# Kernel optimization log

Hardware: AMD Instinct MI355X
Metric: run time of the kernel (lower is better)

The kernel has to match this reference:

```python
import jax, jax.numpy as jnp
import numpy as np

B, L, D, H = 2, 2048, 1024, 16
HD = D // H


def setup_inputs() -> dict:
    key = jax.random.key(0)
    ks = jax.random.split(key, 5)
    # xavier-uniform-ish scale for DxD linears
    scale = float(np.sqrt(6.0 / (D + D)))
    def lin_w(k):
        return jax.random.uniform(k, (D, D), jnp.float32, -scale, scale)
    return {
        "x": jax.random.normal(ks[0], (B, L, D), jnp.float32),
        "wq": lin_w(ks[1]), "bq": jnp.zeros((D,), jnp.float32),
        "wk": lin_w(ks[2]), "bk": jnp.zeros((D,), jnp.float32),
        "wv": lin_w(ks[3]), "bv": jnp.zeros((D,), jnp.float32),
        "wo": lin_w(ks[4]), "bo": jnp.zeros((D,), jnp.float32),
    }


def reference(x, wq, bq, wk, bk, wv, bv, wo, bo):
    b, l, d = x.shape
    # projections: torch Linear is x @ W.T + b
    def split_heads(t):
        return t.reshape(b, l, H, HD).transpose(0, 2, 1, 3)  # (B,H,L,HD)
    Q = split_heads(x @ wq.T + bq)
    K = split_heads(x @ wk.T + bk)
    V = split_heads(x @ wv.T + bv)
    scores = jnp.einsum("bhqd,bhkd->bhqk", Q, K) / jnp.sqrt(jnp.asarray(HD, x.dtype))
    attn = jax.nn.softmax(scores, axis=-1)  # (B,H,L,L)
    out = jnp.einsum("bhqk,bhkd->bhqd", attn, V)
    out = out.transpose(0, 2, 1, 3).reshape(b, l, d)
    return out @ wo.T + bo
```

## Files before the change

### kernel.cpp

```cpp
#include <hip/hip_runtime.h>
#include <hip/hip_bf16.h>
#include <cstdint>

#define LEN   2048
#define DMODEL 1024
#define NH    16
#define HD    64
#define BH    32
#define MROWS 4096

typedef __attribute__((ext_vector_type(8))) short bf16x8;
typedef __attribute__((ext_vector_type(4))) float f32x4;
typedef __attribute__((ext_vector_type(16))) float f32x16;
typedef unsigned int u32;

__device__ __forceinline__ void gload_lds16(const void* g, void* l) {
    __builtin_amdgcn_global_load_lds(
        (const __attribute__((address_space(1))) u32*)g,
        (__attribute__((address_space(3))) u32*)l, 16, 0, 0);
}

__device__ __forceinline__ unsigned short bfb(float f) {
    __hip_bfloat16 h = __float2bfloat16(f);
    return *reinterpret_cast<unsigned short*>(&h);
}

__device__ __forceinline__ u32 pk2(float lo, float hi) {
    return (u32)bfb(lo) | ((u32)bfb(hi) << 16);
}

__global__ void cast_all_k(const float* __restrict__ x,
                           const float* __restrict__ wq, const float* __restrict__ wk,
                           const float* __restrict__ wv, const float* __restrict__ wo,
                           __hip_bfloat16* __restrict__ x_bf,
                           __hip_bfloat16* __restrict__ wqkv,
                           __hip_bfloat16* __restrict__ wo_bf) {
    constexpr int XC = 1048576;
    constexpr int WC = 262144;
    constexpr int TC = XC + 4 * WC;
    int stride = gridDim.x * blockDim.x;
    for (int i = blockIdx.x * blockDim.x + threadIdx.x; i < TC; i += stride) {
        const float* src; __hip_bfloat16* dst; int so, do_;
        if (i < XC) { src = x; dst = x_bf; so = i; do_ = i; }
        else {
            int j = i - XC, w = j >> 18, o = j & (WC - 1);
            src = w == 0 ? wq : (w == 1 ? wk : (w == 2 ? wv : wo));
            so = o;
            if (w < 3) { dst = wqkv; do_ = j; }
            else       { dst = wo_bf; do_ = o; }
        }
        float4 v = reinterpret_cast<const float4*>(src)[so];
        ushort4 p;
        p.x = bfb(v.x); p.y = bfb(v.y); p.z = bfb(v.z); p.w = bfb(v.w);
        reinterpret_cast<ushort4*>(dst)[do_] = p;
    }
}

__global__ __launch_bounds__(256) void gemm_qkv(
    const __hip_bfloat16* __restrict__ A,
    const __hip_bfloat16* __restrict__ Bw,
    const float* __restrict__ bq, const float* __restrict__ bk,
    const float* __restrict__ bv,
    __hip_bfloat16* __restrict__ Qb, __hip_bfloat16* __restrict__ Kb,
    __hip_bfloat16* __restrict__ VTb) {
    constexpr int Kd = DMODEL;
    __shared__ __hip_bfloat16 As[128 * 32];
    __shared__ __hip_bfloat16 Bs[128 * 32];
    const int lin = blockIdx.x;
    const int wg = (lin & 7) * 96 + (lin >> 3);
    const int by = wg / 24, bx = wg % 24;
    const int tid = threadIdx.x;
    const int wave = tid >> 6, lane = tid & 63;
    const int lg = lane >> 4, lr = lane & 15;
    const int wr = wave >> 1, wc = wave & 1;
    const __hip_bfloat16* Ab = A + (size_t)by * 128 * Kd;
    const __hip_bfloat16* Bb = Bw + (size_t)bx * 128 * Kd;
    f32x4 acc[4][4] = {};
    for (int kt = 0; kt < Kd / 32; ++kt) {
#pragma unroll
        for (int i = 0; i < 2; ++i) {
            int c = tid + i * 256;
            int row = c >> 2, c4 = c & 3;
            gload_lds16(Ab + (size_t)row * Kd + kt * 32 + c4 * 8, &As[c * 8]);
        }
#pragma unroll
        for (int i = 0; i < 2; ++i) {
            int c = tid + i * 256;
            int row = c >> 2, c4 = c & 3;
            gload_lds16(Bb + (size_t)row * Kd + kt * 32 + c4 * 8, &Bs[c * 8]);
        }
        __syncthreads();
        bf16x8 af[4], bfr[4];
#pragma unroll
        for (int m = 0; m < 4; ++m)
            af[m] = *(const bf16x8*)&As[(wr * 64 + m * 16 + lr) * 32 + lg * 8];
#pragma unroll
        for (int n = 0; n < 4; ++n)
            bfr[n] = *(const bf16x8*)&Bs[(wc * 64 + n * 16 + lr) * 32 + lg * 8];
        __builtin_amdgcn_s_setprio(1);
#pragma unroll
        for (int m = 0; m < 4; ++m)
#pragma unroll
            for (int n = 0; n < 4; ++n)
                acc[m][n] = __builtin_amdgcn_mfma_f32_16x16x32_bf16(
                    af[m], bfr[n], acc[m][n], 0, 0, 0);
        __builtin_amdgcn_s_setprio(0);
        __syncthreads();
    }
    const int sel = (bx * 128) >> 10;
    const float* bp = sel == 0 ? bq : (sel == 1 ? bk : bv);
    __hip_bfloat16* dst = sel == 0 ? Qb : (sel == 1 ? Kb : VTb);
#pragma unroll
    for (int m = 0; m < 4; ++m)
#pragma unroll
        for (int n = 0; n < 4; ++n)
#pragma unroll
            for (int r = 0; r < 4; ++r) {
                int gm = by * 128 + wr * 64 + m * 16 + lg * 4 + r;
                int gn = bx * 128 + wc * 64 + n * 16 + lr;
                int nn = gn & (DMODEL - 1);
                float v = acc[m][n][r] + bp[nn];
                int bb = gm >> 11, l = gm & (LEN - 1);
                int h = nn >> 6, hd = nn & (HD - 1);
                size_t addr = (sel < 2)
                    ? ((((size_t)bb * NH + h) * LEN + l) * HD + hd)
                    : ((((size_t)bb * NH + h) * HD + hd) * LEN + l);
                dst[addr] = __float2bfloat16(v);
            }
}

#define SC 0.18033688f
__global__ __launch_bounds__(256) void attn_fwd(
    const __hip_bfloat16* __restrict__ Qb,
    const __hip_bfloat16* __restrict__ Kb,
    const __hip_bfloat16* __restrict__ VTb,
    __hip_bfloat16* __restrict__ Ob) {
    const int lin = blockIdx.x;
    const int wg = (lin & 7) * 64 + (lin >> 3);
    const int bh = wg >> 4;
    const int qt = wg & 15;
    const int b = bh >> 4, h = bh & (NH - 1);
    const int tid = threadIdx.x;
    const int wave = tid >> 6, lane = tid & 63;
    const int l31 = lane & 31, hi = lane >> 5;
    const int qw = qt * 128 + wave * 32;
    const __hip_bfloat16* Qp = Qb + ((size_t)bh * LEN + qw) * HD;
    const __hip_bfloat16* Kp = Kb + (size_t)bh * LEN * HD;
    const __hip_bfloat16* Vp = VTb + (size_t)bh * HD * LEN;

    __shared__ __hip_bfloat16 Ks[2][64 * 64];
    __shared__ __hip_bfloat16 Vs[2][64 * 64];
    __shared__ __hip_bfloat16 Pl[4][32][72];
    __hip_bfloat16* prow = &Pl[wave][l31][0];

    const int c0 = tid, c1 = tid + 256;
    const int r0 = c0 >> 3, j0 = (c0 & 7) ^ (r0 & 7);
    const int r1 = c1 >> 3, j1 = (c1 & 7) ^ (r1 & 7);
    const __hip_bfloat16* kg0 = Kp + (size_t)r0 * HD + j0 * 8;
    const __hip_bfloat16* kg1 = Kp + (size_t)r1 * HD + j1 * 8;
    const __hip_bfloat16* vg0 = Vp + (size_t)r0 * LEN + j0 * 8;
    const __hip_bfloat16* vg1 = Vp + (size_t)r1 * LEN + j1 * 8;

    bf16x8 qf[4];
#pragma unroll
    for (int ks = 0; ks < 4; ++ks)
        qf[ks] = *(const bf16x8*)(Qp + l31 * HD + ks * 16 + hi * 8);

    float m_i = -INFINITY;
    float l_i = 0.f;
    f32x16 o[2] = {};

    gload_lds16(kg0, &Ks[0][c0 * 8]);
    gload_lds16(kg1, &Ks[0][c1 * 8]);
    gload_lds16(vg0, &Vs[0][c0 * 8]);
    gload_lds16(vg1, &Vs[0][c1 * 8]);
    __syncthreads();

    const int swz = l31 & 7;
    constexpr int NT = LEN / 64;
    for (int kt = 0; kt < NT; ++kt) {
        const int cb = kt & 1, nb = cb ^ 1;
        if (kt + 1 < NT) {
            size_t ko = (size_t)(kt + 1) * 64 * HD;
            size_t vo = (size_t)(kt + 1) * 64;
            gload_lds16(kg0 + ko, &Ks[nb][c0 * 8]);
            gload_lds16(kg1 + ko, &Ks[nb][c1 * 8]);
            gload_lds16(vg0 + vo, &Vs[nb][c0 * 8]);
            gload_lds16(vg1 + vo, &Vs[nb][c1 * 8]);
        }
        const __hip_bfloat16* ksp = Ks[cb];
        const __hip_bfloat16* vsp = Vs[cb];
        f32x16 s0 = {}, s1 = {};
        __builtin_amdgcn_s_setprio(1);
#pragma unroll
        for (int ks = 0; ks < 4; ++ks) {
            int ch = ((ks << 1) + hi);
            bf16x8 kf0 = *(const bf16x8*)&ksp[l31 * 64 + (ch ^ swz) * 8];
            bf16x8 kf1 = *(const bf16x8*)&ksp[(32 + l31) * 64 + (ch ^ swz) * 8];
            s0 = __builtin_amdgcn_mfma_f32_32x32x16_bf16(kf0, qf[ks], s0, 0, 0, 0);
            s1 = __builtin_amdgcn_mfma_f32_32x32x16_bf16(kf1, qf[ks], s1, 0, 0, 0);
        }
        __builtin_amdgcn_s_setprio(0);
        float mx[16];
#pragma unroll
        for (int r = 0; r < 16; ++r) mx[r] = fmaxf(s0[r], s1[r]);
#pragma unroll
        for (int st = 8; st > 0; st >>= 1)
#pragma unroll
            for (int r = 0; r < 8; ++r)
                if (r < st) mx[r] = fmaxf(mx[r], mx[r + st]);
        float tmax = fmaxf(mx[0], __shfl_xor(mx[0], 32, 64));
        float pmax = tmax * SC;
        if (__any(pmax > m_i + 8.f)) {
            float mnew = fmaxf(m_i, pmax);
            float corr = exp2f(m_i - mnew);
            m_i = mnew;
            l_i *= corr;
#pragma unroll
            for (int r = 0; r < 16; ++r) {
                float cr = __shfl(corr, (r & 3) + 8 * (r >> 2) + 4 * hi, 32);
                o[0][r] *= cr;
                o[1][r] *= cr;
            }
        }
#pragma unroll
        for (int r = 0; r < 16; ++r) {
            s0[r] = exp2f(s0[r] * SC - m_i);
            s1[r] = exp2f(s1[r] * SC - m_i);
        }
        float sm[16];
#pragma unroll
        for (int r = 0; r < 16; ++r) sm[r] = s0[r] + s1[r];
#pragma unroll
        for (int st = 8; st > 0; st >>= 1)
#pragma unroll
            for (int r = 0; r < 8; ++r)
                if (r < st) sm[r] += sm[r + st];
        l_i += sm[0] + __shfl_xor(sm[0], 32, 64);
#pragma unroll
        for (int g = 0; g < 4; ++g) {
            uint2 w0, w1;
            w0.x = pk2(s0[4 * g + 0], s0[4 * g + 1]);
            w0.y = pk2(s0[4 * g + 2], s0[4 * g + 3]);
            w1.x = pk2(s1[4 * g + 0], s1[4 * g + 1]);
            w1.y = pk2(s1[4 * g + 2], s1[4 * g + 3]);
            *(uint2*)&prow[8 * g + 4 * hi]      = w0;
            *(uint2*)&prow[32 + 8 * g + 4 * hi] = w1;
        }
        asm volatile("" ::: "memory");
        bf16x8 pa[4];
#pragma unroll
        for (int ks = 0; ks < 4; ++ks)
            pa[ks] = *(const bf16x8*)&prow[ks * 16 + hi * 8];
        __builtin_amdgcn_s_setprio(1);
#pragma unroll
        for (int ks = 0; ks < 4; ++ks) {
            int ch = ((ks << 1) + hi);
            bf16x8 vf0 = *(const bf16x8*)&vsp[l31 * 64 + (ch ^ swz) * 8];
            bf16x8 vf1 = *(const bf16x8*)&vsp[(32 + l31) * 64 + (ch ^ swz) * 8];
            o[0] = __builtin_amdgcn_mfma_f32_32x32x16_bf16(pa[ks], vf0, o[0], 0, 0, 0);
            o[1] = __builtin_amdgcn_mfma_f32_32x32x16_bf16(pa[ks], vf1, o[1], 0, 0, 0);
        }
        __builtin_amdgcn_s_setprio(0);
        __syncthreads();
    }
#pragma unroll
    for (int r = 0; r < 16; ++r) {
        int q = (r & 3) + 8 * (r >> 2) + 4 * hi;
        float inv = 1.f / __shfl(l_i, q, 32);
        int gq = qw + q;
        size_t base = ((size_t)b * LEN + gq) * DMODEL + h * HD + l31;
        Ob[base]      = __float2bfloat16(o[0][r] * inv);
        Ob[base + 32] = __float2bfloat16(o[1][r] * inv);
    }
}

__global__ __launch_bounds__(256) void gemm_out(
    const __hip_bfloat16* __restrict__ A,
    const __hip_bfloat16* __restrict__ Bw,
    const float* __restrict__ bo, float* __restrict__ out) {
    constexpr int Kd = DMODEL, N = DMODEL;
    __shared__ __hip_bfloat16 As[128 * 32];
    __shared__ __hip_bfloat16 Bs[128 * 32];
    const int lin = blockIdx.x;
    const int wg = (lin & 7) * 32 + (lin >> 3);
    const int by = wg >> 3, bx = wg & 7;
    const int tid = threadIdx.x;
    const int wave = tid >> 6, lane = tid & 63;
    const int lg = lane >> 4, lr = lane & 15;
    const int wr = wave >> 1, wc = wave & 1;
    const __hip_bfloat16* Ab = A + (size_t)by * 128 * Kd;
    const __hip_bfloat16* Bb = Bw + (size_t)bx * 128 * Kd;
    f32x4 acc[4][4] = {};
    for (int kt = 0; kt < Kd / 32; ++kt) {
#pragma unroll
        for (int i = 0; i < 2; ++i) {
            int c = tid + i * 256;
            int row = c >> 2, c4 = c & 3;
            gload_lds16(Ab + (size_t)row * Kd + kt * 32 + c4 * 8, &As[c * 8]);
        }
#pragma unroll
        for (int i = 0; i < 2; ++i) {
            int c = tid + i * 256;
            int row = c >> 2, c4 = c & 3;
            gload_lds16(Bb + (size_t)row * Kd + kt * 32 + c4 * 8, &Bs[c * 8]);
        }
        __syncthreads();
        bf16x8 af[4], bfr[4];
#pragma unroll
        for (int m = 0; m < 4; ++m)
            af[m] = *(const bf16x8*)&As[(wr * 64 + m * 16 + lr) * 32 + lg * 8];
#pragma unroll
        for (int n = 0; n < 4; ++n)
            bfr[n] = *(const bf16x8*)&Bs[(wc * 64 + n * 16 + lr) * 32 + lg * 8];
        __builtin_amdgcn_s_setprio(1);
#pragma unroll
        for (int m = 0; m < 4; ++m)
#pragma unroll
            for (int n = 0; n < 4; ++n)
                acc[m][n] = __builtin_amdgcn_mfma_f32_16x16x32_bf16(
                    af[m], bfr[n], acc[m][n], 0, 0, 0);
        __builtin_amdgcn_s_setprio(0);
        __syncthreads();
    }
#pragma unroll
    for (int m = 0; m < 4; ++m)
#pragma unroll
        for (int n = 0; n < 4; ++n)
#pragma unroll
            for (int r = 0; r < 4; ++r) {
                int gm = by * 128 + wr * 64 + m * 16 + lg * 4 + r;
                int gn = bx * 128 + wc * 64 + n * 16 + lr;
                out[(size_t)gm * N + gn] = acc[m][n][r] + bo[gn];
            }
}

extern "C" void kernel_launch(void* const* d_in, const int* in_sizes, int n_in,
                              void* d_out, int out_size, void* d_ws, size_t ws_size,
                              hipStream_t stream) {
    const float* x  = (const float*)d_in[0];
    const float* wq = (const float*)d_in[1];
    const float* bq = (const float*)d_in[2];
    const float* wk = (const float*)d_in[3];
    const float* bk = (const float*)d_in[4];
    const float* wv = (const float*)d_in[5];
    const float* bv = (const float*)d_in[6];
    const float* wo = (const float*)d_in[7];
    const float* bo = (const float*)d_in[8];

    char* ws = (char*)d_ws;
    __hip_bfloat16* x_bf  = (__hip_bfloat16*)(ws);
    __hip_bfloat16* wqkv  = (__hip_bfloat16*)(ws + (8u  << 20));
    __hip_bfloat16* wo_bf = (__hip_bfloat16*)(ws + (14u << 20));
    __hip_bfloat16* Qb    = (__hip_bfloat16*)(ws + (16u << 20));
    __hip_bfloat16* Kb    = (__hip_bfloat16*)(ws + (24u << 20));
    __hip_bfloat16* VTb   = (__hip_bfloat16*)(ws + (32u << 20));
    __hip_bfloat16* Ob    = (__hip_bfloat16*)(ws + (40u << 20));

    cast_all_k<<<1024, 256, 0, stream>>>(x, wq, wk, wv, wo, x_bf, wqkv, wo_bf);
    gemm_qkv<<<768, 256, 0, stream>>>(x_bf, wqkv, bq, bk, bv, Qb, Kb, VTb);
    attn_fwd<<<512, 256, 0, stream>>>(Qb, Kb, VTb, Ob);
    gemm_out<<<256, 256, 0, stream>>>(Ob, wo_bf, bo, (float*)d_out);
}
```

Measured before the change: 228.8 us.

## Split attention KV tile across wave pairs and double-buffer GEMM LDS loads

The attention kernel now runs 8 waves per block. Each pair of waves shares a 32-query strip and splits every 64-key tile into two halves, each keeping its own running max and sum. The two partial results are merged through shared memory at the end. Both GEMM kernels gain double-buffered LDS tiles so the next K-slice load overlaps the current MFMAs, removing one barrier per iteration. The cost is larger LDS use per block, an extra reduction step, and lower occupancy from the larger attention blocks.

After: 223.5 us. 1.02x faster.

```diff
diff --git a/kernel.cpp b/kernel.cpp
--- a/kernel.cpp
+++ b/kernel.cpp
@@ -64,8 +64,8 @@
     __hip_bfloat16* __restrict__ Qb, __hip_bfloat16* __restrict__ Kb,
     __hip_bfloat16* __restrict__ VTb) {
     constexpr int Kd = DMODEL;
-    __shared__ __hip_bfloat16 As[128 * 32];
-    __shared__ __hip_bfloat16 Bs[128 * 32];
+    __shared__ __hip_bfloat16 As[2][128 * 32];
+    __shared__ __hip_bfloat16 Bs[2][128 * 32];
     const int lin = blockIdx.x;
     const int wg = (lin & 7) * 96 + (lin >> 3);
     const int by = wg / 24, bx = wg % 24;
@@ -75,28 +75,31 @@
     const int wr = wave >> 1, wc = wave & 1;
     const __hip_bfloat16* Ab = A + (size_t)by * 128 * Kd;
     const __hip_bfloat16* Bb = Bw + (size_t)bx * 128 * Kd;
+    const int c0 = tid, c1 = tid + 256;
+    const int ra0 = c0 >> 2, ca0 = c0 & 3;
+    const int ra1 = c1 >> 2, ca1 = c1 & 3;
     f32x4 acc[4][4] = {};
+    gload_lds16(Ab + (size_t)ra0 * Kd + ca0 * 8, &As[0][c0 * 8]);
+    gload_lds16(Ab + (size_t)ra1 * Kd + ca1 * 8, &As[0][c1 * 8]);
+    gload_lds16(Bb + (size_t)ra0 * Kd + ca0 * 8, &Bs[0][c0 * 8]);
+    gload_lds16(Bb + (size_t)ra1 * Kd + ca1 * 8, &Bs[0][c1 * 8]);
+    __syncthreads();
     for (int kt = 0; kt < Kd / 32; ++kt) {
-#pragma unroll
-        for (int i = 0; i < 2; ++i) {
-            int c = tid + i * 256;
-            int row = c >> 2, c4 = c & 3;
-            gload_lds16(Ab + (size_t)row * Kd + kt * 32 + c4 * 8, &As[c * 8]);
-        }
-#pragma unroll
-        for (int i = 0; i < 2; ++i) {
-            int c = tid + i * 256;
-            int row = c >> 2, c4 = c & 3;
-            gload_lds16(Bb + (size_t)row * Kd + kt * 32 + c4 * 8, &Bs[c * 8]);
-        }
-        __syncthreads();
+        const int cb = kt & 1, nb = cb ^ 1;
+        if (kt + 1 < Kd / 32) {
+            int ko = (kt + 1) * 32;
+            gload_lds16(Ab + (size_t)ra0 * Kd + ko + ca0 * 8, &As[nb][c0 * 8]);
+            gload_lds16(Ab + (size_t)ra1 * Kd + ko + ca1 * 8, &As[nb][c1 * 8]);
+            gload_lds16(Bb + (size_t)ra0 * Kd + ko + ca0 * 8, &Bs[nb][c0 * 8]);
+            gload_lds16(Bb + (size_t)ra1 * Kd + ko + ca1 * 8, &Bs[nb][c1 * 8]);
+        }
         bf16x8 af[4], bfr[4];
 #pragma unroll
         for (int m = 0; m < 4; ++m)
-            af[m] = *(const bf16x8*)&As[(wr * 64 + m * 16 + lr) * 32 + lg * 8];
+            af[m] = *(const bf16x8*)&As[cb][(wr * 64 + m * 16 + lr) * 32 + lg * 8];
 #pragma unroll
         for (int n = 0; n < 4; ++n)
-            bfr[n] = *(const bf16x8*)&Bs[(wc * 64 + n * 16 + lr) * 32 + lg * 8];
+            bfr[n] = *(const bf16x8*)&Bs[cb][(wc * 64 + n * 16 + lr) * 32 + lg * 8];
         __builtin_amdgcn_s_setprio(1);
 #pragma unroll
         for (int m = 0; m < 4; ++m)
@@ -130,7 +133,7 @@
 }
 
 #define SC 0.18033688f
-__global__ __launch_bounds__(256) void attn_fwd(
+__global__ __launch_bounds__(512) void attn_fwd(
     const __hip_bfloat16* __restrict__ Qb,
     const __hip_bfloat16* __restrict__ Kb,
     const __hip_bfloat16* __restrict__ VTb,
@@ -143,23 +146,22 @@
     const int tid = threadIdx.x;
     const int wave = tid >> 6, lane = tid & 63;
     const int l31 = lane & 31, hi = lane >> 5;
-    const int qw = qt * 128 + wave * 32;
+    const int strip = wave >> 1, kh = wave & 1;
+    const int qw = qt * 128 + strip * 32;
     const __hip_bfloat16* Qp = Qb + ((size_t)bh * LEN + qw) * HD;
     const __hip_bfloat16* Kp = Kb + (size_t)bh * LEN * HD;
     const __hip_bfloat16* Vp = VTb + (size_t)bh * HD * LEN;
 
-    __shared__ __hip_bfloat16 Ks[2][64 * 64];
-    __shared__ __hip_bfloat16 Vs[2][64 * 64];
-    __shared__ __hip_bfloat16 Pl[4][32][72];
-    __hip_bfloat16* prow = &Pl[wave][l31][0];
-
-    const int c0 = tid, c1 = tid + 256;
+    __shared__ alignas(16) char smem[53248];
+    __hip_bfloat16* KsB = (__hip_bfloat16*)smem;
+    __hip_bfloat16* VsB = (__hip_bfloat16*)(smem + 16384);
+    __hip_bfloat16* PlB = (__hip_bfloat16*)(smem + 32768);
+    __hip_bfloat16* prow = PlB + (wave * 32 + l31) * 40;
+
+    const int c0 = tid;
     const int r0 = c0 >> 3, j0 = (c0 & 7) ^ (r0 & 7);
-    const int r1 = c1 >> 3, j1 = (c1 & 7) ^ (r1 & 7);
     const __hip_bfloat16* kg0 = Kp + (size_t)r0 * HD + j0 * 8;
-    const __hip_bfloat16* kg1 = Kp + (size_t)r1 * HD + j1 * 8;
     const __hip_bfloat16* vg0 = Vp + (size_t)r0 * LEN + j0 * 8;
-    const __hip_bfloat16* vg1 = Vp + (size_t)r1 * LEN + j1 * 8;
 
     bf16x8 qf[4];
 #pragma unroll
@@ -168,12 +170,10 @@
 
     float m_i = -INFINITY;
     float l_i = 0.f;
-    f32x16 o[2] = {};
-
-    gload_lds16(kg0, &Ks[0][c0 * 8]);
-    gload_lds16(kg1, &Ks[0][c1 * 8]);
-    gload_lds16(vg0, &Vs[0][c0 * 8]);
-    gload_lds16(vg1, &Vs[0][c1 * 8]);
+    f32x16 o0 = {}, o1 = {};
+
+    gload_lds16(kg0, &KsB[c0 * 8]);
+    gload_lds16(vg0, &VsB[c0 * 8]);
     __syncthreads();
 
     const int swz = l31 & 7;
@@ -181,29 +181,23 @@
     for (int kt = 0; kt < NT; ++kt) {
         const int cb = kt & 1, nb = cb ^ 1;
         if (kt + 1 < NT) {
-            size_t ko = (size_t)(kt + 1) * 64 * HD;
-            size_t vo = (size_t)(kt + 1) * 64;
-            gload_lds16(kg0 + ko, &Ks[nb][c0 * 8]);
-            gload_lds16(kg1 + ko, &Ks[nb][c1 * 8]);
-            gload_lds16(vg0 + vo, &Vs[nb][c0 * 8]);
-            gload_lds16(vg1 + vo, &Vs[nb][c1 * 8]);
-        }
-        const __hip_bfloat16* ksp = Ks[cb];
-        const __hip_bfloat16* vsp = Vs[cb];
-        f32x16 s0 = {}, s1 = {};
+            gload_lds16(kg0 + (size_t)(kt + 1) * 64 * HD, &KsB[nb * 4096 + c0 * 8]);
+            gload_lds16(vg0 + (size_t)(kt + 1) * 64,      &VsB[nb * 4096 + c0 * 8]);
+        }
+        const __hip_bfloat16* ksp = KsB + cb * 4096;
+        const __hip_bfloat16* vsp = VsB + cb * 4096;
+        f32x16 s = {};
         __builtin_amdgcn_s_setprio(1);
 #pragma unroll
         for (int ks = 0; ks < 4; ++ks) {
-            int ch = ((ks << 1) + hi);
-            bf16x8 kf0 = *(const bf16x8*)&ksp[l31 * 64 + (ch ^ swz) * 8];
-            bf16x8 kf1 = *(const bf16x8*)&ksp[(32 + l31) * 64 + (ch ^ swz) * 8];
-            s0 = __builtin_amdgcn_mfma_f32_32x32x16_bf16(kf0, qf[ks], s0, 0, 0, 0);
-            s1 = __builtin_amdgcn_mfma_f32_32x32x16_bf16(kf1, qf[ks], s1, 0, 0, 0);
+            int ch = (ks << 1) + hi;
+            bf16x8 kf = *(const bf16x8*)&ksp[(kh * 32 + l31) * 64 + ((ch ^ swz)) * 8];
+            s = __builtin_amdgcn_mfma_f32_32x32x16_bf16(kf, qf[ks], s, 0, 0, 0);
         }
         __builtin_amdgcn_s_setprio(0);
         float mx[16];
 #pragma unroll
-        for (int r = 0; r < 16; ++r) mx[r] = fmaxf(s0[r], s1[r]);
+        for (int r = 0; r < 16; ++r) mx[r] = s[r];
 #pragma unroll
         for (int st = 8; st > 0; st >>= 1)
 #pragma unroll
@@ -219,18 +213,15 @@
 #pragma unroll
             for (int r = 0; r < 16; ++r) {
                 float cr = __shfl(corr, (r & 3) + 8 * (r >> 2) + 4 * hi, 32);
-                o[0][r] *= cr;
-                o[1][r] *= cr;
+                o0[r] *= cr;
+                o1[r] *= cr;
             }
         }
 #pragma unroll
-        for (int r = 0; r < 16; ++r) {
-            s0[r] = exp2f(s0[r] * SC - m_i);
-            s1[r] = exp2f(s1[r] * SC - m_i);
-        }
+        for (int r = 0; r < 16; ++r) s[r] = exp2f(s[r] * SC - m_i);
         float sm[16];
 #pragma unroll
-        for (int r = 0; r < 16; ++r) sm[r] = s0[r] + s1[r];
+        for (int r = 0; r < 16; ++r) sm[r] = s[r];
 #pragma unroll
         for (int st = 8; st > 0; st >>= 1)
 #pragma unroll
@@ -239,39 +230,64 @@
         l_i += sm[0] + __shfl_xor(sm[0], 32, 64);
 #pragma unroll
         for (int g = 0; g < 4; ++g) {
-            uint2 w0, w1;
-            w0.x = pk2(s0[4 * g + 0], s0[4 * g + 1]);
-            w0.y = pk2(s0[4 * g + 2], s0[4 * g + 3]);
-            w1.x = pk2(s1[4 * g + 0], s1[4 * g + 1]);
-            w1.y = pk2(s1[4 * g + 2], s1[4 * g + 3]);
-            *(uint2*)&prow[8 * g + 4 * hi]      = w0;
-            *(uint2*)&prow[32 + 8 * g + 4 * hi] = w1;
+            uint2 w;
+            w.x = pk2(s[4 * g + 0], s[4 * g + 1]);
+            w.y = pk2(s[4 * g + 2], s[4 * g + 3]);
+            *(uint2*)&prow[8 * g + 4 * hi] = w;
         }
         asm volatile("" ::: "memory");
-        bf16x8 pa[4];
-#pragma unroll
-        for (int ks = 0; ks < 4; ++ks)
-            pa[ks] = *(const bf16x8*)&prow[ks * 16 + hi * 8];
+        bf16x8 pa0 = *(const bf16x8*)&prow[hi * 8];
+        bf16x8 pa1 = *(const bf16x8*)&prow[16 + hi * 8];
         __builtin_amdgcn_s_setprio(1);
 #pragma unroll
-        for (int ks = 0; ks < 4; ++ks) {
-            int ch = ((ks << 1) + hi);
-            bf16x8 vf0 = *(const bf16x8*)&vsp[l31 * 64 + (ch ^ swz) * 8];
-            bf16x8 vf1 = *(const bf16x8*)&vsp[(32 + l31) * 64 + (ch ^ swz) * 8];
-            o[0] = __builtin_amdgcn_mfma_f32_32x32x16_bf16(pa[ks], vf0, o[0], 0, 0, 0);
-            o[1] = __builtin_amdgcn_mfma_f32_32x32x16_bf16(pa[ks], vf1, o[1], 0, 0, 0);
+        for (int ks2 = 0; ks2 < 2; ++ks2) {
+            int ch = kh * 4 + (ks2 << 1) + hi;
+            bf16x8 pa = ks2 == 0 ? pa0 : pa1;
+            bf16x8 vf0 = *(const bf16x8*)&vsp[l31 * 64 + ((ch ^ swz)) * 8];
+            bf16x8 vf1 = *(const bf16x8*)&vsp[(32 + l31) * 64 + ((ch ^ swz)) * 8];
+            o0 = __builtin_amdgcn_mfma_f32_32x32x16_bf16(pa, vf0, o0, 0, 0, 0);
+            o1 = __builtin_amdgcn_mfma_f32_32x32x16_bf16(pa, vf1, o1, 0, 0, 0);
         }
         __builtin_amdgcn_s_setprio(0);
         __syncthreads();
     }
+    float* MO = (float*)smem;
+    float* ML = (float*)(smem + 34816);
+    ML[((strip * 2 + kh) * 32 + l31) * 2 + 0] = m_i;
+    ML[((strip * 2 + kh) * 32 + l31) * 2 + 1] = l_i;
+    __syncthreads();
+    float w_own[16], w_inv[16];
 #pragma unroll
     for (int r = 0; r < 16; ++r) {
         int q = (r & 3) + 8 * (r >> 2) + 4 * hi;
-        float inv = 1.f / __shfl(l_i, q, 32);
-        int gq = qw + q;
-        size_t base = ((size_t)b * LEN + gq) * DMODEL + h * HD + l31;
-        Ob[base]      = __float2bfloat16(o[0][r] * inv);
-        Ob[base + 32] = __float2bfloat16(o[1][r] * inv);
+        float m0 = ML[((strip * 2 + 0) * 32 + q) * 2 + 0];
+        float l0 = ML[((strip * 2 + 0) * 32 + q) * 2 + 1];
+        float m1 = ML[((strip * 2 + 1) * 32 + q) * 2 + 0];
+        float l1 = ML[((strip * 2 + 1) * 32 + q) * 2 + 1];
+        float m = fmaxf(m0, m1);
+        float w0 = exp2f(m0 - m), w1 = exp2f(m1 - m);
+        w_own[r] = (kh == 0) ? w0 : w1;
+        w_inv[r] = 1.f / (l0 * w0 + l1 * w1);
+    }
+    if (kh == 1) {
+#pragma unroll
+        for (int r = 0; r < 16; ++r) {
+            MO[(strip * 64 + lane) * 33 + r]      = o0[r] * w_own[r];
+            MO[(strip * 64 + lane) * 33 + 16 + r] = o1[r] * w_own[r];
+        }
+    }
+    __syncthreads();
+    if (kh == 0) {
+#pragma unroll
+        for (int r = 0; r < 16; ++r) {
+            int q = (r & 3) + 8 * (r >> 2) + 4 * hi;
+            int gq = qw + q;
+            size_t base = ((size_t)b * LEN + gq) * DMODEL + h * HD + l31;
+            float v0 = (o0[r] * w_own[r] + MO[(strip * 64 + lane) * 33 + r]) * w_inv[r];
+            float v1 = (o1[r] * w_own[r] + MO[(strip * 64 + lane) * 33 + 16 + r]) * w_inv[r];
+            Ob[base]      = __float2bfloat16(v0);
+            Ob[base + 32] = __float2bfloat16(v1);
+        }
     }
 }
 
@@ -280,8 +296,8 @@
     const __hip_bfloat16* __restrict__ Bw,
     const float* __restrict__ bo, float* __restrict__ out) {
     constexpr int Kd = DMODEL, N = DMODEL;
-    __shared__ __hip_bfloat16 As[128 * 32];
-    __shared__ __hip_bfloat16 Bs[128 * 32];
+    __shared__ __hip_bfloat16 As[2][128 * 32];
+    __shared__ __hip_bfloat16 Bs[2][128 * 32];
     const int lin = blockIdx.x;
     const int wg = (lin & 7) * 32 + (lin >> 3);
     const int by = wg >> 3, bx = wg & 7;
@@ -291,28 +307,31 @@
     const int wr = wave >> 1, wc = wave & 1;
     const __hip_bfloat16* Ab = A + (size_t)by * 128 * Kd;
     const __hip_bfloat16* Bb = Bw + (size_t)bx * 128 * Kd;
+    const int c0 = tid, c1 = tid + 256;
+    const int ra0 = c0 >> 2, ca0 = c0 & 3;
+    const int ra1 = c1 >> 2, ca1 = c1 & 3;
     f32x4 acc[4][4] = {};
+    gload_lds16(Ab + (size_t)ra0 * Kd + ca0 * 8, &As[0][c0 * 8]);
+    gload_lds16(Ab + (size_t)ra1 * Kd + ca1 * 8, &As[0][c1 * 8]);
+    gload_lds16(Bb + (size_t)ra0 * Kd + ca0 * 8, &Bs[0][c0 * 8]);
+    gload_lds16(Bb + (size_t)ra1 * Kd + ca1 * 8, &Bs[0][c1 * 8]);
+    __syncthreads();
     for (int kt = 0; kt < Kd / 32; ++kt) {
-#pragma unroll
-        for (int i = 0; i < 2; ++i) {
-            int c = tid + i * 256;
-            int row = c >> 2, c4 = c & 3;
-            gload_lds16(Ab + (size_t)row * Kd + kt * 32 + c4 * 8, &As[c * 8]);
-        }
-#pragma unroll
-        for (int i = 0; i < 2; ++i) {
-            int c = tid + i * 256;
-            int row = c >> 2, c4 = c & 3;
-            gload_lds16(Bb + (size_t)row * Kd + kt * 32 + c4 * 8, &Bs[c * 8]);
-        }
-        __syncthreads();
+        const int cb = kt & 1, nb = cb ^ 1;
+        if (kt + 1 < Kd / 32) {
+            int ko = (kt + 1) * 32;
+            gload_lds16(Ab + (size_t)ra0 * Kd + ko + ca0 * 8, &As[nb][c0 * 8]);
+            gload_lds16(Ab + (size_t)ra1 * Kd + ko + ca1 * 8, &As[nb][c1 * 8]);
+            gload_lds16(Bb + (size_t)ra0 * Kd + ko + ca0 * 8, &Bs[nb][c0 * 8]);
+            gload_lds16(Bb + (size_t)ra1 * Kd + ko + ca1 * 8, &Bs[nb][c1 * 8]);
+        }
         bf16x8 af[4], bfr[4];
 #pragma unroll
         for (int m = 0; m < 4; ++m)
-            af[m] = *(const bf16x8*)&As[(wr * 64 + m * 16 + lr) * 32 + lg * 8];
+            af[m] = *(const bf16x8*)&As[cb][(wr * 64 + m * 16 + lr) * 32 + lg * 8];
 #pragma unroll
         for (int n = 0; n < 4; ++n)
-            bfr[n] = *(const bf16x8*)&Bs[(wc * 64 + n * 16 + lr) * 32 + lg * 8];
+            bfr[n] = *(const bf16x8*)&Bs[cb][(wc * 64 + n * 16 + lr) * 32 + lg * 8];
         __builtin_amdgcn_s_setprio(1);
 #pragma unroll
         for (int m = 0; m < 4; ++m)
@@ -359,6 +378,6 @@
 
     cast_all_k<<<1024, 256, 0, stream>>>(x, wq, wk, wv, wo, x_bf, wqkv, wo_bf);
     gemm_qkv<<<768, 256, 0, stream>>>(x_bf, wqkv, bq, bk, bv, Qb, Kb, VTb);
-    attn_fwd<<<512, 256, 0, stream>>>(Qb, Kb, VTb, Ob);
+    attn_fwd<<<512, 512, 0, stream>>>(Qb, Kb, VTb, Ob);
     gemm_out<<<256, 256, 0, stream>>>(Ob, wo_bf, bo, (float*)d_out);
 }
```
